# Performance work log

Measured on AMD Instinct MI355X. Metric: run time of the kernel, lower is better.

Reference implementation:

```python
import jax, jax.numpy as jnp
import numpy as np

EMBED_DIM = 1024
N_HEADS = 16
HEAD_DIM = EMBED_DIM // N_HEADS
MAX_REL_POS = 2  # hardcoded in the torch module


def _rel_index(length_q, length_k):
    # final_mat[i, j] = clip(i - j, -p, p) + p  with i over k-range, j over q-range
    rq = jnp.arange(length_q)[None, :]
    rk = jnp.arange(length_k)[:, None]
    dist = jnp.clip(rk - rq, -MAX_REL_POS, MAX_REL_POS) + MAX_REL_POS
    return dist  # (len_k, len_q) int; square when len_q == len_k


def setup_inputs() -> dict:
    key = jax.random.key(0)
    ks = jax.random.split(key, 16)
    B, S, E, H, D = 4, 1024, EMBED_DIM, N_HEADS, HEAD_DIM
    xavier = lambda k, shape: jax.random.uniform(
        k, shape, jnp.float32, -1.0, 1.0) * np.sqrt(6.0 / (shape[0] + shape[1]))
    return {
        "query": jax.random.normal(ks[0], (B, S, E), jnp.float32),
        "key": jax.random.normal(ks[1], (B, S, E), jnp.float32),
        "value": jax.random.normal(ks[2], (B, S, E), jnp.float32),
        "Wq": xavier(ks[3], (E, E)), "bq": jnp.zeros((E,), jnp.float32),
        "Wk": xavier(ks[4], (E, E)), "bk": jnp.zeros((E,), jnp.float32),
        "Wv": xavier(ks[5], (E, E)), "bv": jnp.zeros((E,), jnp.float32),
        "Wo": xavier(ks[6], (E, E)), "bo": jnp.zeros((E,), jnp.float32),
        "rpk_table": xavier(ks[7], (2 * MAX_REL_POS + 1, D)),
        "rpv_table": xavier(ks[8], (2 * MAX_REL_POS + 1, D)),
    }


def reference(query, key, value, Wq, bq, Wk, bk, Wv, bv, Wo, bo, rpk_table, rpv_table):
    B, S, E = query.shape
    H, D = N_HEADS, HEAD_DIM
    q = query @ Wq.T + bq
    _k = key @ Wk.T + bk      # computed but unused (faithful to source bug)
    v = value @ Wv.T + bv

    qh = q.reshape(B, S, H, D).transpose(0, 2, 1, 3)   # b h s d
    vh = v.reshape(B, S, H, D).transpose(0, 2, 1, 3)

    # NOTE: source uses query for both sides of the dot product
    dots = jnp.einsum('bhqd,bhkd->bhqk', qh, qh)

    idx = _rel_index(S, S)                              # (S, S)
    rpk = rpk_table[idx]                                # (S, S, D)
    rp_dots = jnp.einsum('bhqd,qkd->bhqk', qh, rpk)

    scale = jnp.sqrt(jnp.asarray(D, q.dtype))
    attn = jax.nn.softmax((dots + rp_dots) / scale, axis=-1)

    weight1 = jnp.einsum('bhqk,bhkd->bhqd', attn, vh)
    rpv = rpv_table[idx]                                # (S, S, D)
    weight2 = jnp.einsum('bhqk,qkd->bhqd', attn, rpv)

    out = (weight1 + weight2).transpose(0, 2, 1, 3).reshape(B, S, E)
    return out @ Wo.T + bo
```

## Files before the change

### kernel.cpp

```cpp
#include <hip/hip_runtime.h>


typedef _Float16 v8h __attribute__((ext_vector_type(8)));
typedef _Float16 v4h __attribute__((ext_vector_type(4)));
typedef float    v4f __attribute__((ext_vector_type(4)));

#define MFMA_F16(A_, B_, C_) __builtin_amdgcn_mfma_f32_16x16x32_f16(A_, B_, C_, 0, 0, 0)

__device__ __forceinline__ void async_copy16(const void* g, void* l) {
    __builtin_amdgcn_global_load_lds(
        (const __attribute__((address_space(1))) void*)g,
        (__attribute__((address_space(3))) void*)l, 16, 0, 0);
}

__global__ __launch_bounds__(256) void cvt5_kernel(
    const float* __restrict__ s0, const float* __restrict__ s1,
    const float* __restrict__ s2, const float* __restrict__ s3,
    const float* __restrict__ s4,
    _Float16* __restrict__ d0, _Float16* __restrict__ d1,
    _Float16* __restrict__ d2, _Float16* __restrict__ d3,
    _Float16* __restrict__ d4,
    int n0, int n1, int n2, int n3, int n4)
{
    const float* s; _Float16* d; int n;
    switch (blockIdx.y) {
        case 0:  s = s0; d = d0; n = n0; break;
        case 1:  s = s1; d = d1; n = n1; break;
        case 2:  s = s2; d = d2; n = n2; break;
        case 3:  s = s3; d = d3; n = n3; break;
        default: s = s4; d = d4; n = n4; break;
    }
    int i = (blockIdx.x * 256 + threadIdx.x) * 4;
    if (i >= n) return;
    float4 f = *(const float4*)(s + i);
    v4h o = { (_Float16)f.x, (_Float16)f.y, (_Float16)f.z, (_Float16)f.w };
    *(v4h*)(d + i) = o;
}

template<int TM>
__device__ __forceinline__ void gemm_core(const _Float16* __restrict__ A,
                                          const _Float16* __restrict__ W,
                                          const float* __restrict__ bias,
                                          int mode, void* __restrict__ outp)
{
    __shared__ __align__(16) _Float16 smem[2 * 128 * 64];
    _Float16* As = smem;
    _Float16* Bs = smem + 128 * 64;

    const int tid  = threadIdx.x;
    const int wave = tid >> 6, lane = tid & 63;
    const int quad = lane >> 4, n16 = lane & 15;
    const int wm = (TM == 128) ? (wave >> 1) : 0;
    const int wn = (TM == 128) ? (wave & 1) : wave;
    const int WCOLS = (TM == 128) ? 64 : 32;
    const int NJ = WCOLS / 16;
    const int row0 = blockIdx.y * TM, col0 = blockIdx.x * 128;
    const int rL = lane >> 3, c8 = lane & 7;
    const int lcs = c8 ^ rL;

    v4f acc[4][4] = {};

    for (int kb = 0; kb < 1024; kb += 64) {
        __syncthreads();
        #pragma unroll
        for (int p = 0; p < TM / 32; p++) {
            int rg = wave * (TM / 32) + p;
            int row = rg * 8 + rL;
            async_copy16(A + (size_t)(row0 + row) * 1024 + kb + lcs * 8, &As[rg * 512]);
        }
        #pragma unroll
        for (int p = 0; p < 4; p++) {
            int rg = wave * 4 + p;
            int row = rg * 8 + rL;
            async_copy16(W + (size_t)(col0 + row) * 1024 + kb + lcs * 8, &Bs[rg * 512]);
        }
        __syncthreads();
        #pragma unroll
        for (int ks = 0; ks < 64; ks += 32) {
            const int pc = ((ks >> 3) + quad) ^ (n16 & 7);
            v8h af[4], bf[4];
            #pragma unroll
            for (int i = 0; i < 4; i++)
                af[i] = *(const v8h*)(&As[(wm * 64 + i * 16 + n16) * 64 + pc * 8]);
            #pragma unroll
            for (int j = 0; j < NJ; j++)
                bf[j] = *(const v8h*)(&Bs[(wn * WCOLS + j * 16 + n16) * 64 + pc * 8]);
            #pragma unroll
            for (int i = 0; i < 4; i++)
                #pragma unroll
                for (int j = 0; j < NJ; j++)
                    acc[i][j] = MFMA_F16(af[i], bf[j], acc[i][j]);
        }
    }

    __syncthreads();
    char* scb = (char*)smem + wave * 8192;

    const int b     = (row0 + wm * 64) >> 10;
    const int srow0 = (row0 + wm * 64) & 1023;

    if (mode == 0) {
        _Float16* sc = (_Float16*)scb;
        #pragma unroll
        for (int i = 0; i < 4; i++)
            #pragma unroll
            for (int j = 0; j < 4; j++)
                #pragma unroll
                for (int r = 0; r < 4; r++) {
                    int rowL = i * 16 + quad * 4 + r, colL = j * 16 + n16;
                    float v = acc[i][j][r] + bias[col0 + wn * 64 + colL];
                    sc[rowL * 64 + (((colL >> 3) ^ (rowL & 7)) << 3) + (colL & 7)] = (_Float16)v;
                }
        int h = (col0 + wn * 64) >> 6;
        #pragma unroll
        for (int it = 0; it < 8; it++) {
            int rowR = it * 8 + (lane >> 3), cR = lane & 7;
            v8h val = *(const v8h*)(&sc[rowR * 64 + ((cR ^ (rowR & 7)) << 3)]);
            *(v8h*)((_Float16*)outp +
                    (((size_t)(b * 16 + h) * 1024 + srow0 + rowR) << 6) + cR * 8) = val;
        }
    } else if (mode == 1) {
        _Float16* sc = (_Float16*)scb;
        #pragma unroll
        for (int i = 0; i < 4; i++)
            #pragma unroll
            for (int j = 0; j < 4; j++) {
                int colL = j * 16 + n16;
                int c16 = i * 2 + (quad >> 1);
                v4h pk;
                #pragma unroll
                for (int r = 0; r < 4; r++)
                    pk[r] = (_Float16)(acc[i][j][r] + bias[col0 + wn * 64 + colL]);
                *(v4h*)(&sc[colL * 64 + ((c16 ^ (colL & 7)) << 3) + (quad & 1) * 4]) = pk;
            }
        #pragma unroll
        for (int it = 0; it < 8; it++) {
            int dR = it * 8 + (lane >> 3), scn = lane & 7;
            v8h val = *(const v8h*)(&sc[dR * 64 + ((scn ^ (dR & 7)) << 3)]);
            int cg = col0 + wn * 64 + dR;
            int h = cg >> 6, dl = cg & 63;
            *(v8h*)((_Float16*)outp +
                    ((size_t)((b * 16 + h) * 64 + dl) << 10) + srow0 + scn * 8) = val;
        }
    } else {
        float* sc = (float*)scb;
        #pragma unroll
        for (int i = 0; i < 4; i++)
            #pragma unroll
            for (int j = 0; j < 2; j++)
                #pragma unroll
                for (int r = 0; r < 4; r++) {
                    int rowL = i * 16 + quad * 4 + r, colL = j * 16 + n16;
                    sc[rowL * 32 + (((colL >> 2) ^ (rowL & 7)) << 2) + (colL & 3)] =
                        acc[i][j][r] + bias[col0 + wn * 32 + colL];
                }
        #pragma unroll
        for (int it = 0; it < 8; it++) {
            int rowR = it * 8 + (lane >> 3), cR = lane & 7;
            v4f val = *(const v4f*)(&sc[rowR * 32 + ((cR ^ (rowR & 7)) << 2)]);
            *(v4f*)((float*)outp + (size_t)(row0 + rowR) * 1024 + col0 + wn * 32 + cR * 4) = val;
        }
    }
}

__global__ __launch_bounds__(256) void gemm_qv_kernel(
    const _Float16* __restrict__ Aq, const _Float16* __restrict__ Av,
    const _Float16* __restrict__ Wq, const _Float16* __restrict__ Wv,
    const float* __restrict__ bq, const float* __restrict__ bv,
    _Float16* __restrict__ q_out, _Float16* __restrict__ v_out)
{
    int z = blockIdx.z;
    gemm_core<128>(z ? Av : Aq, z ? Wv : Wq, z ? bv : bq, z ? 1 : 0,
                   z ? (void*)v_out : (void*)q_out);
}

__global__ __launch_bounds__(256) void gemm_o_kernel(
    const _Float16* __restrict__ A, const _Float16* __restrict__ W,
    const float* __restrict__ bias, float* __restrict__ outp)
{
    gemm_core<64>(A, W, bias, 2, (void*)outp);
}

__global__ __launch_bounds__(256) void attn_kernel(
    const _Float16* __restrict__ qb,
    const _Float16* __restrict__ vt,
    const float* __restrict__ rpk, const float* __restrict__ rpv,
    _Float16* __restrict__ attn_o)
{
    const int blk = blockIdx.x;
    const int bh = blk & 63;
    const int q0 = (blk >> 6) * 64;
    const int tid = threadIdx.x;
    const int wave = tid >> 6, lane = tid & 63;
    const int quad = lane >> 4, n16 = lane & 15;
    const int qw = q0 + wave * 16;
    const _Float16* Qh = qb + (size_t)bh * 1024 * 64;
    const _Float16* Vh = vt + (size_t)bh * 64 * 1024;

    __shared__ __align__(16) _Float16 Ks[64 * 64];
    __shared__ __align__(16) _Float16 Vs[64 * 64];
    __shared__ __align__(16) _Float16 Ps[4][16 * 64];
    __shared__ float rqs[4][16][5];

    {
        int m = lane >> 2, seg = lane & 3;
        const _Float16* qrow = Qh + (size_t)(qw + m) * 64 + seg * 16;
        v8h qa = *(const v8h*)(qrow);
        v8h qc = *(const v8h*)(qrow + 8);
        float qd[16];
        #pragma unroll
        for (int x = 0; x < 8; x++) { qd[x] = (float)qa[x]; qd[8 + x] = (float)qc[x]; }
        float qq = 0.f;
        #pragma unroll
        for (int x = 0; x < 16; x++) qq += qd[x] * qd[x];
        qq += __shfl_xor(qq, 1);
        qq += __shfl_xor(qq, 2);
        #pragma unroll
        for (int t = 0; t < 5; t++) {
            float s = 0.f;
            #pragma unroll
            for (int x = 0; x < 16; x++) s += qd[x] * rpk[t * 64 + seg * 16 + x];
            s += __shfl_xor(s, 1);
            s += __shfl_xor(s, 2);
            if (seg == 0) rqs[wave][m][t] = (s - qq) * 0.125f;
        }
    }
    __syncthreads();

    float rc[5];
    #pragma unroll
    for (int t = 0; t < 5; t++) rc[t] = rqs[wave][n16][t];

    v8h aq0 = *(const v8h*)(Qh + (size_t)(qw + n16) * 64 + quad * 8);
    v8h aq1 = *(const v8h*)(Qh + (size_t)(qw + n16) * 64 + 32 + quad * 8);

    float bkt[5] = {0.f, 0.f, 0.f, 0.f, 0.f};
    v4f O[4] = {};

    const int rL = lane >> 3, c8 = lane & 7;
    const int lcs = c8 ^ rL;
    const int pphys0 = quad ^ (n16 & 7);
    const int pphys1 = (quad + 4) ^ (n16 & 7);

    for (int kb = 0; kb < 1024; kb += 64) {
        __syncthreads();
        #pragma unroll
        for (int p = 0; p < 2; p++) {
            int c = wave * 2 + p;
            int row = c * 8 + rL;
            async_copy16(Qh + (size_t)(kb + row) * 64 + lcs * 8, &Ks[c * 512]);
            async_copy16(Vh + (size_t)row * 1024 + kb + lcs * 8, &Vs[c * 512]);
        }
        __syncthreads();

        #pragma unroll
        for (int t = 0; t < 4; t++) {
            v8h ak0 = *(const v8h*)(&Ks[(t * 16 + n16) * 64 + pphys0 * 8]);
            v8h ak1 = *(const v8h*)(&Ks[(t * 16 + n16) * 64 + pphys1 * 8]);
            v4f s = {0.f, 0.f, 0.f, 0.f};
            s = MFMA_F16(ak0, aq0, s);
            s = MFMA_F16(ak1, aq1, s);
            const int dqt = qw - kb - t * 16;
            float pv[4];
            if (dqt >= 32) {
                #pragma unroll
                for (int r = 0; r < 4; r++) {
                    float p = __expf(fmaf(s[r], 0.125f, rc[4]));
                    pv[r] = p; bkt[4] += p;
                }
            } else if (dqt <= -32) {
                #pragma unroll
                for (int r = 0; r < 4; r++) {
                    float p = __expf(fmaf(s[r], 0.125f, rc[0]));
                    pv[r] = p; bkt[0] += p;
                }
            } else {
                #pragma unroll
                for (int r = 0; r < 4; r++) {
                    int diff = dqt + n16 - quad * 4 - r;
                    float rv = diff >= 2  ? rc[4]
                             : diff == 1  ? rc[3]
                             : diff == 0  ? rc[2]
                             : diff == -1 ? rc[1]
                                          : rc[0];
                    float p = __expf(fmaf(s[r], 0.125f, rv));
                    pv[r] = p;
                    bkt[4] += (diff >= 2)  ? p : 0.f;
                    bkt[3] += (diff == 1)  ? p : 0.f;
                    bkt[2] += (diff == 0)  ? p : 0.f;
                    bkt[1] += (diff == -1) ? p : 0.f;
                    bkt[0] += (diff <= -2) ? p : 0.f;
                }
            }
            v4h pk = { (_Float16)pv[0], (_Float16)pv[1], (_Float16)pv[2], (_Float16)pv[3] };
            int c16 = t * 2 + (quad >> 1);
            *(v4h*)(&Ps[wave][n16 * 64 + ((c16 ^ (n16 & 7)) << 3) + (quad & 1) * 4]) = pk;
        }

        v8h pf0 = *(const v8h*)(&Ps[wave][n16 * 64 + pphys0 * 8]);
        v8h pf1 = *(const v8h*)(&Ps[wave][n16 * 64 + pphys1 * 8]);
        #pragma unroll
        for (int dt = 0; dt < 4; dt++) {
            v8h av0 = *(const v8h*)(&Vs[(dt * 16 + n16) * 64 + pphys0 * 8]);
            v8h av1 = *(const v8h*)(&Vs[(dt * 16 + n16) * 64 + pphys1 * 8]);
            O[dt] = MFMA_F16(av0, pf0, O[dt]);
            O[dt] = MFMA_F16(av1, pf1, O[dt]);
        }
    }

    #pragma unroll
    for (int t = 0; t < 5; t++) {
        bkt[t] += __shfl_xor(bkt[t], 16);
        bkt[t] += __shfl_xor(bkt[t], 32);
    }
    float l = bkt[0] + bkt[1] + bkt[2] + bkt[3] + bkt[4];
    float inv = 1.0f / l;
    int q = qw + n16;
    size_t orow = (size_t)((bh >> 4) * 1024 + q) * 1024 + (bh & 15) * 64;
    #pragma unroll
    for (int dt = 0; dt < 4; dt++) {
        int d0 = dt * 16 + quad * 4;
        v4h st;
        #pragma unroll
        for (int r = 0; r < 4; r++) {
            int d = d0 + r;
            float w2 = bkt[4] * rpv[4 * 64 + d] + bkt[3] * rpv[3 * 64 + d]
                     + bkt[2] * rpv[2 * 64 + d] + bkt[1] * rpv[1 * 64 + d]
                     + bkt[0] * rpv[0 * 64 + d];
            st[r] = (_Float16)((O[dt][r] + w2) * inv);
        }
        *(v4h*)(attn_o + orow + d0) = st;
    }
}

extern "C" void kernel_launch(void* const* d_in, const int* in_sizes, int n_in,
                              void* d_out, int out_size, void* d_ws, size_t ws_size,
                              hipStream_t stream)
{
    const float* query = (const float*)d_in[0];
    const float* value = (const float*)d_in[2];
    const float* Wq = (const float*)d_in[3];
    const float* bq = (const float*)d_in[4];
    const float* Wv = (const float*)d_in[7];
    const float* bv = (const float*)d_in[8];
    const float* Wo = (const float*)d_in[9];
    const float* bo = (const float*)d_in[10];
    const float* rpk = (const float*)d_in[11];
    const float* rpv = (const float*)d_in[12];
    float* out = (float*)d_out;

    char* ws = (char*)d_ws;
    const size_t MB = 1024 * 1024;
    _Float16* q_bhsd = (_Float16*)(ws);
    _Float16* v_t    = (_Float16*)(ws + 8 * MB);
    _Float16* q16    = (_Float16*)(ws + 16 * MB);
    _Float16* attn_o = (_Float16*)(ws + 16 * MB);
    _Float16* v16    = (_Float16*)(ws + 24 * MB);
    _Float16* wq16   = (_Float16*)(ws + 32 * MB);
    _Float16* wv16   = (_Float16*)(ws + 34 * MB);
    _Float16* wo16   = (_Float16*)(ws + 36 * MB);

    cvt5_kernel<<<dim3(4096, 5), 256, 0, stream>>>(
        query, value, Wq, Wv, Wo, q16, v16, wq16, wv16, wo16,
        4096 * 1024, 4096 * 1024, 1024 * 1024, 1024 * 1024, 1024 * 1024);

    gemm_qv_kernel<<<dim3(8, 32, 2), 256, 0, stream>>>(
        q16, v16, wq16, wv16, bq, bv, q_bhsd, v_t);

    attn_kernel<<<dim3(1024), 256, 0, stream>>>(q_bhsd, v_t, rpk, rpv, attn_o);

    gemm_o_kernel<<<dim3(8, 64), 256, 0, stream>>>(attn_o, wo16, bo, out);
}
```

Before: 203.4 us.

## Double-buffer K/V tiles in LDS and pass P through lane shuffles

```diff
diff --git a/kernel.cpp b/kernel.cpp
--- a/kernel.cpp
+++ b/kernel.cpp
@@ -3,6 +3,7 @@
 
 typedef _Float16 v8h __attribute__((ext_vector_type(8)));
 typedef _Float16 v4h __attribute__((ext_vector_type(4)));
+typedef _Float16 v2h __attribute__((ext_vector_type(2)));
 typedef float    v4f __attribute__((ext_vector_type(4)));
 
 #define MFMA_F16(A_, B_, C_) __builtin_amdgcn_mfma_f32_16x16x32_f16(A_, B_, C_, 0, 0, 0)
@@ -197,10 +198,22 @@
     const _Float16* Qh = qb + (size_t)bh * 1024 * 64;
     const _Float16* Vh = vt + (size_t)bh * 64 * 1024;
 
-    __shared__ __align__(16) _Float16 Ks[64 * 64];
-    __shared__ __align__(16) _Float16 Vs[64 * 64];
-    __shared__ __align__(16) _Float16 Ps[4][16 * 64];
+    __shared__ __align__(16) _Float16 Ks[2][64 * 64];
+    __shared__ __align__(16) _Float16 Vs[2][64 * 64];
     __shared__ float rqs[4][16][5];
+
+    const int rL = lane >> 3, c8 = lane & 7;
+    const int lcs = c8 ^ rL;
+
+    {
+        #pragma unroll
+        for (int p = 0; p < 2; p++) {
+            int c = wave * 2 + p;
+            int row = c * 8 + rL;
+            async_copy16(Qh + (size_t)row * 64 + lcs * 8, &Ks[0][c * 512]);
+            async_copy16(Vh + (size_t)row * 1024 + lcs * 8, &Vs[0][c * 512]);
+        }
+    }
 
     {
         int m = lane >> 2, seg = lane & 3;
@@ -225,38 +238,45 @@
             if (seg == 0) rqs[wave][m][t] = (s - qq) * 0.125f;
         }
     }
+
+    v8h aq0 = *(const v8h*)(Qh + (size_t)(qw + n16) * 64 + quad * 8);
+    v8h aq1 = *(const v8h*)(Qh + (size_t)(qw + n16) * 64 + 32 + quad * 8);
+
     __syncthreads();
 
     float rc[5];
     #pragma unroll
     for (int t = 0; t < 5; t++) rc[t] = rqs[wave][n16][t];
 
-    v8h aq0 = *(const v8h*)(Qh + (size_t)(qw + n16) * 64 + quad * 8);
-    v8h aq1 = *(const v8h*)(Qh + (size_t)(qw + n16) * 64 + 32 + quad * 8);
-
     float bkt[5] = {0.f, 0.f, 0.f, 0.f, 0.f};
     v4f O[4] = {};
 
-    const int rL = lane >> 3, c8 = lane & 7;
-    const int lcs = c8 ^ rL;
     const int pphys0 = quad ^ (n16 & 7);
     const int pphys1 = (quad + 4) ^ (n16 & 7);
-
-    for (int kb = 0; kb < 1024; kb += 64) {
-        __syncthreads();
-        #pragma unroll
-        for (int p = 0; p < 2; p++) {
-            int c = wave * 2 + p;
-            int row = c * 8 + rL;
-            async_copy16(Qh + (size_t)(kb + row) * 64 + lcs * 8, &Ks[c * 512]);
-            async_copy16(Vh + (size_t)row * 1024 + kb + lcs * 8, &Vs[c * 512]);
-        }
-        __syncthreads();
-
+    const int srcA = ((quad & 1) << 5) + n16;
+    const int srcB = srcA + 16;
+    const bool tHi = (quad >> 1) != 0;
+
+    for (int it = 0; it < 16; ++it) {
+        const int cur = it & 1;
+        const int kb = it * 64;
+        if (it + 1 < 16) {
+            const int nxt = 1 - cur;
+            const int kn = kb + 64;
+            #pragma unroll
+            for (int p = 0; p < 2; p++) {
+                int c = wave * 2 + p;
+                int row = c * 8 + rL;
+                async_copy16(Qh + (size_t)(kn + row) * 64 + lcs * 8, &Ks[nxt][c * 512]);
+                async_copy16(Vh + (size_t)row * 1024 + kn + lcs * 8, &Vs[nxt][c * 512]);
+            }
+        }
+
+        int pkLo[4], pkHi[4];
         #pragma unroll
         for (int t = 0; t < 4; t++) {
-            v8h ak0 = *(const v8h*)(&Ks[(t * 16 + n16) * 64 + pphys0 * 8]);
-            v8h ak1 = *(const v8h*)(&Ks[(t * 16 + n16) * 64 + pphys1 * 8]);
+            v8h ak0 = *(const v8h*)(&Ks[cur][(t * 16 + n16) * 64 + pphys0 * 8]);
+            v8h ak1 = *(const v8h*)(&Ks[cur][(t * 16 + n16) * 64 + pphys1 * 8]);
             v4f s = {0.f, 0.f, 0.f, 0.f};
             s = MFMA_F16(ak0, aq0, s);
             s = MFMA_F16(ak1, aq1, s);
@@ -292,20 +312,34 @@
                     bkt[0] += (diff <= -2) ? p : 0.f;
                 }
             }
-            v4h pk = { (_Float16)pv[0], (_Float16)pv[1], (_Float16)pv[2], (_Float16)pv[3] };
-            int c16 = t * 2 + (quad >> 1);
-            *(v4h*)(&Ps[wave][n16 * 64 + ((c16 ^ (n16 & 7)) << 3) + (quad & 1) * 4]) = pk;
-        }
-
-        v8h pf0 = *(const v8h*)(&Ps[wave][n16 * 64 + pphys0 * 8]);
-        v8h pf1 = *(const v8h*)(&Ps[wave][n16 * 64 + pphys1 * 8]);
+            pkLo[t] = __builtin_bit_cast(int, __builtin_amdgcn_cvt_pkrtz(pv[0], pv[1]));
+            pkHi[t] = __builtin_bit_cast(int, __builtin_amdgcn_cvt_pkrtz(pv[2], pv[3]));
+        }
+
+        int aL0 = __shfl(pkLo[0], srcA), aH0 = __shfl(pkHi[0], srcA);
+        int bL0 = __shfl(pkLo[0], srcB), bH0 = __shfl(pkHi[0], srcB);
+        int aL1 = __shfl(pkLo[1], srcA), aH1 = __shfl(pkHi[1], srcA);
+        int bL1 = __shfl(pkLo[1], srcB), bH1 = __shfl(pkHi[1], srcB);
+        int aL2 = __shfl(pkLo[2], srcA), aH2 = __shfl(pkHi[2], srcA);
+        int bL2 = __shfl(pkLo[2], srcB), bH2 = __shfl(pkHi[2], srcB);
+        int aL3 = __shfl(pkLo[3], srcA), aH3 = __shfl(pkHi[3], srcA);
+        int bL3 = __shfl(pkLo[3], srcB), bH3 = __shfl(pkHi[3], srcB);
+        union { int d[4]; v8h v; } u0, u1;
+        u0.d[0] = tHi ? aL1 : aL0;  u0.d[1] = tHi ? aH1 : aH0;
+        u0.d[2] = tHi ? bL1 : bL0;  u0.d[3] = tHi ? bH1 : bH0;
+        u1.d[0] = tHi ? aL3 : aL2;  u1.d[1] = tHi ? aH3 : aH2;
+        u1.d[2] = tHi ? bL3 : bL2;  u1.d[3] = tHi ? bH3 : bH2;
+        v8h pf0 = u0.v, pf1 = u1.v;
+
         #pragma unroll
         for (int dt = 0; dt < 4; dt++) {
-            v8h av0 = *(const v8h*)(&Vs[(dt * 16 + n16) * 64 + pphys0 * 8]);
-            v8h av1 = *(const v8h*)(&Vs[(dt * 16 + n16) * 64 + pphys1 * 8]);
+            v8h av0 = *(const v8h*)(&Vs[cur][(dt * 16 + n16) * 64 + pphys0 * 8]);
+            v8h av1 = *(const v8h*)(&Vs[cur][(dt * 16 + n16) * 64 + pphys1 * 8]);
             O[dt] = MFMA_F16(av0, pf0, O[dt]);
             O[dt] = MFMA_F16(av1, pf1, O[dt]);
         }
+
+        __syncthreads();
     }
 
     #pragma unroll
```

Result: slower. 209.3 us (+2.9%).
